# Performance work log

Measured on AMD Instinct MI355X. Metric: run time of the kernel, lower is better.

Reference implementation:

```python
import jax, jax.numpy as jnp
import numpy as np

COST_CLASS = 1.0
COST_BBOX = 5.0
COST_GIOU = 2.0
EPS = 1e-6

BS, Q, T = 8, 900, 256   # batch, num_queries, max_text_len
M = 2000                 # total target boxes concatenated over batch


def setup_inputs() -> dict:
    key = jax.random.key(0)
    k1, k2, k3, k4 = jax.random.split(key, 4)
    pred_logits = jax.random.normal(k1, (BS, Q, T), dtype=jnp.float32)
    pred_boxes = jax.random.uniform(k2, (BS, Q, 4), dtype=jnp.float32, minval=0.05, maxval=0.95)
    tgt_boxes = jax.random.uniform(k3, (M, 4), dtype=jnp.float32, minval=0.05, maxval=0.95)
    tgt_labels = jax.random.uniform(k4, (M, T), dtype=jnp.float32)  # positive token map (soft)
    return {"pred_logits": pred_logits, "pred_boxes": pred_boxes,
            "tgt_boxes": tgt_boxes, "tgt_labels": tgt_labels}


def box_cxcywh_to_xyxy(b):
    cx, cy, w, h = b[..., 0], b[..., 1], b[..., 2], b[..., 3]
    return jnp.stack([cx - 0.5 * w, cy - 0.5 * h, cx + 0.5 * w, cy + 0.5 * h], axis=-1)


def generalized_box_iou(boxes1, boxes2):
    # boxes1: [N,4] xyxy, boxes2: [M,4] xyxy -> [N,M] GIoU
    area1 = (boxes1[:, 2] - boxes1[:, 0]) * (boxes1[:, 3] - boxes1[:, 1])
    area2 = (boxes2[:, 2] - boxes2[:, 0]) * (boxes2[:, 3] - boxes2[:, 1])
    lt = jnp.maximum(boxes1[:, None, :2], boxes2[None, :, :2])  # [N,M,2]
    rb = jnp.minimum(boxes1[:, None, 2:], boxes2[None, :, 2:])
    wh = jnp.clip(rb - lt, 0.0)
    inter = wh[..., 0] * wh[..., 1]
    union = area1[:, None] + area2[None, :] - inter
    iou = inter / (union + EPS)
    lt_e = jnp.minimum(boxes1[:, None, :2], boxes2[None, :, :2])
    rb_e = jnp.maximum(boxes1[:, None, 2:], boxes2[None, :, 2:])
    wh_e = jnp.clip(rb_e - lt_e, 0.0)
    area_e = wh_e[..., 0] * wh_e[..., 1]
    return iou - (area_e - union) / (area_e + EPS)


def reference(pred_logits, pred_boxes, tgt_boxes, tgt_labels):
    bs, q, t = pred_logits.shape
    out_prob = jnp.clip(jax.nn.sigmoid(pred_logits.reshape(bs * q, t)), EPS, 1.0 - EPS)
    pred_bbox = pred_boxes.reshape(bs * q, 4)
    # normalized positive token map
    norm_labels = tgt_labels / (jnp.sum(tgt_labels, axis=1, keepdims=True) + EPS)
    # classification cost: -sum_t p[n,t] * map[m,t]  -> [N, M]
    cost_class = -jnp.einsum('nt,mt->nm', out_prob, norm_labels)
    # L1 box cost (cdist p=1) on cxcywh
    cost_bbox = jnp.sum(jnp.abs(pred_bbox[:, None, :] - tgt_boxes[None, :, :]), axis=-1)
    # GIoU cost on xyxy, clamped to >= -1
    giou = generalized_box_iou(box_cxcywh_to_xyxy(pred_bbox), box_cxcywh_to_xyxy(tgt_boxes))
    cost_giou = -jnp.clip(giou, -1.0)
    C = COST_BBOX * cost_bbox + COST_CLASS * cost_class + COST_GIOU * cost_giou
    return C.reshape(bs, q, -1)
```

## Files before the change

### kernel.cpp

```cpp
#include <hip/hip_runtime.h>
#include <math.h>

#define EPSF 1e-6f

typedef __attribute__((ext_vector_type(8))) short bf16x8;
typedef __attribute__((ext_vector_type(4))) float f32x4;
typedef __attribute__((ext_vector_type(4))) unsigned short u16x4;
typedef __attribute__((ext_vector_type(8))) unsigned short u16x8;

constexpr int TT = 256, MT = 2000, NP = 7200;

static __device__ __forceinline__ unsigned short f2bf(float f) {
    unsigned int u = __float_as_uint(f);
    u += 0x7FFFu + ((u >> 16) & 1u);
    return (unsigned short)(u >> 16);
}
static __device__ __forceinline__ float frcp(float x) { return __builtin_amdgcn_rcpf(x); }

__global__ __launch_bounds__(256) void sigmoid_bf16_kernel(const float* __restrict__ in,
                                                           unsigned short* __restrict__ out) {
    int i = (blockIdx.x * 256 + threadIdx.x) * 8;
    float4 x0 = *reinterpret_cast<const float4*>(in + i);
    float4 x1 = *reinterpret_cast<const float4*>(in + i + 4);
    float v[8] = {x0.x, x0.y, x0.z, x0.w, x1.x, x1.y, x1.z, x1.w};
    u16x8 o;
#pragma unroll
    for (int j = 0; j < 8; ++j) {
        float s = frcp(1.0f + __expf(-v[j]));
        s = fminf(fmaxf(s, EPSF), 1.0f - EPSF);
        o[j] = f2bf(s);
    }
    *reinterpret_cast<u16x8*>(out + i) = o;
}

__global__ __launch_bounds__(256) void normlab_bf16_kernel(const float* __restrict__ lab,
                                                           unsigned short* __restrict__ out) {
    int wave = threadIdx.x >> 6;
    int lane = threadIdx.x & 63;
    int m = blockIdx.x * 4 + wave;
    float4 v = reinterpret_cast<const float4*>(lab)[m * (TT / 4) + lane];
    float s = v.x + v.y + v.z + v.w;
#pragma unroll
    for (int off = 32; off > 0; off >>= 1) s += __shfl_down(s, off);
    float inv = frcp(__shfl(s, 0) + EPSF);
    u16x4 o;
    o[0] = f2bf(v.x * inv); o[1] = f2bf(v.y * inv);
    o[2] = f2bf(v.z * inv); o[3] = f2bf(v.w * inv);
    *reinterpret_cast<u16x4*>(out + m * TT + lane * 4) = o;
}

constexpr int BN = 128, BM = 128, BK = 64;
constexpr int LDT = BK + 8;

__global__ __launch_bounds__(256) void cost_mfma_kernel(
    const unsigned short* __restrict__ A,
    const unsigned short* __restrict__ B,
    const float* __restrict__ pbox,
    const float* __restrict__ tbox,
    float* __restrict__ out)
{
    __shared__ __align__(16) unsigned short As[BN * LDT];
    __shared__ __align__(16) unsigned short Bs[BM * LDT];
    const int tid = threadIdx.x;
    const int n0 = blockIdx.x * BN;
    const int m0 = blockIdx.y * BM;
    const int lane = tid & 63, wave = tid >> 6;
    const int wr = wave & 1, wc = wave >> 1;
    const int fr = lane & 15, quad = lane >> 4;
    const int sc = tid & 7;
    const int sr = tid >> 3;

    f32x4 acc[4][4] = {};

    for (int k0 = 0; k0 < TT; k0 += BK) {
        __syncthreads();
#pragma unroll
        for (int p = 0; p < 4; ++p) {
            int row = sr + p * 32;
            int gn = n0 + row; if (gn > NP - 1) gn = NP - 1;
            bf16x8 va = *reinterpret_cast<const bf16x8*>(&A[gn * TT + k0 + sc * 8]);
            *reinterpret_cast<bf16x8*>(&As[row * LDT + sc * 8]) = va;
            int gm = m0 + row; if (gm > MT - 1) gm = MT - 1;
            bf16x8 vb = *reinterpret_cast<const bf16x8*>(&B[gm * TT + k0 + sc * 8]);
            *reinterpret_cast<bf16x8*>(&Bs[row * LDT + sc * 8]) = vb;
        }
        __syncthreads();
#pragma unroll
        for (int ks = 0; ks < 2; ++ks) {
            bf16x8 af[4], bf[4];
#pragma unroll
            for (int t = 0; t < 4; ++t) {
                af[t] = *reinterpret_cast<const bf16x8*>(
                    &As[(wr * 64 + t * 16 + fr) * LDT + ks * 32 + quad * 8]);
                bf[t] = *reinterpret_cast<const bf16x8*>(
                    &Bs[(wc * 64 + t * 16 + fr) * LDT + ks * 32 + quad * 8]);
            }
#pragma unroll
            for (int ti = 0; ti < 4; ++ti)
#pragma unroll
                for (int tj = 0; tj < 4; ++tj)
                    acc[ti][tj] = __builtin_amdgcn_mfma_f32_16x16x32_bf16(
                        af[ti], bf[tj], acc[ti][tj], 0, 0, 0);
        }
    }

    float bcx[4], bcy[4], bww[4], bhh[4], bx1[4], by1[4], bx2[4], by2[4], areaB[4];
    int mj[4]; bool mv[4];
#pragma unroll
    for (int tj = 0; tj < 4; ++tj) {
        int gm = m0 + wc * 64 + tj * 16 + fr;
        mv[tj] = gm < MT;
        int g = mv[tj] ? gm : MT - 1;
        float4 b = *reinterpret_cast<const float4*>(&tbox[g * 4]);
        bcx[tj] = b.x; bcy[tj] = b.y; bww[tj] = b.z; bhh[tj] = b.w;
        bx1[tj] = b.x - 0.5f * b.z; by1[tj] = b.y - 0.5f * b.w;
        bx2[tj] = b.x + 0.5f * b.z; by2[tj] = b.y + 0.5f * b.w;
        areaB[tj] = (bx2[tj] - bx1[tj]) * (by2[tj] - by1[tj]);
        mj[tj] = gm;
    }

#pragma unroll
    for (int ti = 0; ti < 4; ++ti) {
#pragma unroll
        for (int r = 0; r < 4; ++r) {
            int p = n0 + wr * 64 + ti * 16 + quad * 4 + r;
            if (p >= NP) continue;
            float4 pb = *reinterpret_cast<const float4*>(&pbox[p * 4]);
            float ax1 = pb.x - 0.5f * pb.z, ay1 = pb.y - 0.5f * pb.w;
            float ax2 = pb.x + 0.5f * pb.z, ay2 = pb.y + 0.5f * pb.w;
            float areaA = (ax2 - ax1) * (ay2 - ay1);
#pragma unroll
            for (int tj = 0; tj < 4; ++tj) {
                if (!mv[tj]) continue;
                float l1 = fabsf(pb.x - bcx[tj]) + fabsf(pb.y - bcy[tj]) +
                           fabsf(pb.z - bww[tj]) + fabsf(pb.w - bhh[tj]);
                float ltx = fmaxf(ax1, bx1[tj]), lty = fmaxf(ay1, by1[tj]);
                float rbx = fminf(ax2, bx2[tj]), rby = fminf(ay2, by2[tj]);
                float iw = fmaxf(rbx - ltx, 0.0f), ih = fmaxf(rby - lty, 0.0f);
                float inter = iw * ih;
                float uni = areaA + areaB[tj] - inter;
                float iou = inter * frcp(uni + EPSF);
                float ex1 = fminf(ax1, bx1[tj]), ey1 = fminf(ay1, by1[tj]);
                float ex2 = fmaxf(ax2, bx2[tj]), ey2 = fmaxf(ay2, by2[tj]);
                float ew = fmaxf(ex2 - ex1, 0.0f), eh = fmaxf(ey2 - ey1, 0.0f);
                float areaE = ew * eh;
                float giou = iou - (areaE - uni) * frcp(areaE + EPSF);
                float res = 5.0f * l1 - acc[ti][tj][r] - 2.0f * fmaxf(giou, -1.0f);
                out[p * MT + mj[tj]] = res;
            }
        }
    }
}

extern "C" void kernel_launch(void* const* d_in, const int* in_sizes, int n_in,
                              void* d_out, int out_size, void* d_ws, size_t ws_size,
                              hipStream_t stream) {
    const float* pred_logits = (const float*)d_in[0];
    const float* pred_boxes  = (const float*)d_in[1];
    const float* tgt_boxes   = (const float*)d_in[2];
    const float* tgt_labels  = (const float*)d_in[3];
    float* out = (float*)d_out;

    unsigned short* probs = (unsigned short*)d_ws;
    unsigned short* nlab  = probs + NP * TT;

    sigmoid_bf16_kernel<<<NP * TT / (256 * 8), 256, 0, stream>>>(pred_logits, probs);
    normlab_bf16_kernel<<<MT / 4, 256, 0, stream>>>(tgt_labels, nlab);

    dim3 grid((NP + BN - 1) / BN, (MT + BM - 1) / BM);
    cost_mfma_kernel<<<grid, 256, 0, stream>>>(probs, nlab, pred_boxes, tgt_boxes, out);
}
```

Before: 128.4 us.

## Merge prep kernels and load MFMA operands directly from global memory

Folds the sigmoid and label-normalisation kernels into one launch using block-index ranges, removing one kernel launch. The GEMM main loop drops LDS staging and the two barriers per K-step, and instead has each wave load its MFMA fragments straight from global memory through per-row pointers. This avoids shared-memory traffic and synchronisation but makes the 16-byte fragment loads strided across rows and duplicated between waves, so it leans on L1/L2 caching. The GIoU code also picks up a redundant, odd self-referential ey2 expression that is immediately overwritten.

```diff
diff --git a/kernel.cpp b/kernel.cpp
--- a/kernel.cpp
+++ b/kernel.cpp
@@ -17,40 +17,41 @@
 }
 static __device__ __forceinline__ float frcp(float x) { return __builtin_amdgcn_rcpf(x); }
 
-__global__ __launch_bounds__(256) void sigmoid_bf16_kernel(const float* __restrict__ in,
-                                                           unsigned short* __restrict__ out) {
-    int i = (blockIdx.x * 256 + threadIdx.x) * 8;
-    float4 x0 = *reinterpret_cast<const float4*>(in + i);
-    float4 x1 = *reinterpret_cast<const float4*>(in + i + 4);
-    float v[8] = {x0.x, x0.y, x0.z, x0.w, x1.x, x1.y, x1.z, x1.w};
-    u16x8 o;
+__global__ __launch_bounds__(256) void prep_kernel(const float* __restrict__ logits,
+                                                   const float* __restrict__ lab,
+                                                   unsigned short* __restrict__ probs,
+                                                   unsigned short* __restrict__ nlab) {
+    int b = blockIdx.x;
+    if (b < 900) {
+        int i = (b * 256 + threadIdx.x) * 8;
+        float4 x0 = *reinterpret_cast<const float4*>(logits + i);
+        float4 x1 = *reinterpret_cast<const float4*>(logits + i + 4);
+        float v[8] = {x0.x, x0.y, x0.z, x0.w, x1.x, x1.y, x1.z, x1.w};
+        u16x8 o;
 #pragma unroll
-    for (int j = 0; j < 8; ++j) {
-        float s = frcp(1.0f + __expf(-v[j]));
-        s = fminf(fmaxf(s, EPSF), 1.0f - EPSF);
-        o[j] = f2bf(s);
+        for (int j = 0; j < 8; ++j) {
+            float s = frcp(1.0f + __expf(-v[j]));
+            s = fminf(fmaxf(s, EPSF), 1.0f - EPSF);
+            o[j] = f2bf(s);
+        }
+        *reinterpret_cast<u16x8*>(probs + i) = o;
+    } else {
+        int wave = threadIdx.x >> 6;
+        int lane = threadIdx.x & 63;
+        int m = (b - 900) * 4 + wave;
+        float4 v = reinterpret_cast<const float4*>(lab)[m * (TT / 4) + lane];
+        float s = v.x + v.y + v.z + v.w;
+#pragma unroll
+        for (int off = 32; off > 0; off >>= 1) s += __shfl_down(s, off);
+        float inv = frcp(__shfl(s, 0) + EPSF);
+        u16x4 o;
+        o[0] = f2bf(v.x * inv); o[1] = f2bf(v.y * inv);
+        o[2] = f2bf(v.z * inv); o[3] = f2bf(v.w * inv);
+        *reinterpret_cast<u16x4*>(nlab + m * TT + lane * 4) = o;
     }
-    *reinterpret_cast<u16x8*>(out + i) = o;
 }
 
-__global__ __launch_bounds__(256) void normlab_bf16_kernel(const float* __restrict__ lab,
-                                                           unsigned short* __restrict__ out) {
-    int wave = threadIdx.x >> 6;
-    int lane = threadIdx.x & 63;
-    int m = blockIdx.x * 4 + wave;
-    float4 v = reinterpret_cast<const float4*>(lab)[m * (TT / 4) + lane];
-    float s = v.x + v.y + v.z + v.w;
-#pragma unroll
-    for (int off = 32; off > 0; off >>= 1) s += __shfl_down(s, off);
-    float inv = frcp(__shfl(s, 0) + EPSF);
-    u16x4 o;
-    o[0] = f2bf(v.x * inv); o[1] = f2bf(v.y * inv);
-    o[2] = f2bf(v.z * inv); o[3] = f2bf(v.w * inv);
-    *reinterpret_cast<u16x4*>(out + m * TT + lane * 4) = o;
-}
-
-constexpr int BN = 128, BM = 128, BK = 64;
-constexpr int LDT = BK + 8;
+constexpr int BN = 128, BM = 128;
 
 __global__ __launch_bounds__(256) void cost_mfma_kernel(
     const unsigned short* __restrict__ A,
@@ -59,49 +60,38 @@
     const float* __restrict__ tbox,
     float* __restrict__ out)
 {
-    __shared__ __align__(16) unsigned short As[BN * LDT];
-    __shared__ __align__(16) unsigned short Bs[BM * LDT];
     const int tid = threadIdx.x;
     const int n0 = blockIdx.x * BN;
     const int m0 = blockIdx.y * BM;
     const int lane = tid & 63, wave = tid >> 6;
     const int wr = wave & 1, wc = wave >> 1;
     const int fr = lane & 15, quad = lane >> 4;
-    const int sc = tid & 7;
-    const int sr = tid >> 3;
+
+    const unsigned short* pa[4];
+    const unsigned short* pb[4];
+#pragma unroll
+    for (int t = 0; t < 4; ++t) {
+        int gn = n0 + wr * 64 + t * 16 + fr; if (gn > NP - 1) gn = NP - 1;
+        pa[t] = A + gn * TT + quad * 8;
+        int gm = m0 + wc * 64 + t * 16 + fr; if (gm > MT - 1) gm = MT - 1;
+        pb[t] = B + gm * TT + quad * 8;
+    }
 
     f32x4 acc[4][4] = {};
-
-    for (int k0 = 0; k0 < TT; k0 += BK) {
-        __syncthreads();
+#pragma unroll 2
+    for (int kk = 0; kk < TT; kk += 32) {
+        bf16x8 af[4], bg[4];
 #pragma unroll
-        for (int p = 0; p < 4; ++p) {
-            int row = sr + p * 32;
-            int gn = n0 + row; if (gn > NP - 1) gn = NP - 1;
-            bf16x8 va = *reinterpret_cast<const bf16x8*>(&A[gn * TT + k0 + sc * 8]);
-            *reinterpret_cast<bf16x8*>(&As[row * LDT + sc * 8]) = va;
-            int gm = m0 + row; if (gm > MT - 1) gm = MT - 1;
-            bf16x8 vb = *reinterpret_cast<const bf16x8*>(&B[gm * TT + k0 + sc * 8]);
-            *reinterpret_cast<bf16x8*>(&Bs[row * LDT + sc * 8]) = vb;
+        for (int t = 0; t < 4; ++t) {
+            af[t] = *reinterpret_cast<const bf16x8*>(pa[t] + kk);
+            bg[t] = *reinterpret_cast<const bf16x8*>(pb[t] + kk);
         }
-        __syncthreads();
 #pragma unroll
-        for (int ks = 0; ks < 2; ++ks) {
-            bf16x8 af[4], bf[4];
+        for (int ti = 0; ti < 4; ++ti)
 #pragma unroll
-            for (int t = 0; t < 4; ++t) {
-                af[t] = *reinterpret_cast<const bf16x8*>(
-                    &As[(wr * 64 + t * 16 + fr) * LDT + ks * 32 + quad * 8]);
-                bf[t] = *reinterpret_cast<const bf16x8*>(
-                    &Bs[(wc * 64 + t * 16 + fr) * LDT + ks * 32 + quad * 8]);
-            }
-#pragma unroll
-            for (int ti = 0; ti < 4; ++ti)
-#pragma unroll
-                for (int tj = 0; tj < 4; ++tj)
-                    acc[ti][tj] = __builtin_amdgcn_mfma_f32_16x16x32_bf16(
-                        af[ti], bf[tj], acc[ti][tj], 0, 0, 0);
-        }
+            for (int tj = 0; tj < 4; ++tj)
+                acc[ti][tj] = __builtin_amdgcn_mfma_f32_16x16x32_bf16(
+                    af[ti], bg[tj], acc[ti][tj], 0, 0, 0);
     }
 
     float bcx[4], bcy[4], bww[4], bhh[4], bx1[4], by1[4], bx2[4], by2[4], areaB[4];
@@ -125,15 +115,15 @@
         for (int r = 0; r < 4; ++r) {
             int p = n0 + wr * 64 + ti * 16 + quad * 4 + r;
             if (p >= NP) continue;
-            float4 pb = *reinterpret_cast<const float4*>(&pbox[p * 4]);
-            float ax1 = pb.x - 0.5f * pb.z, ay1 = pb.y - 0.5f * pb.w;
-            float ax2 = pb.x + 0.5f * pb.z, ay2 = pb.y + 0.5f * pb.w;
+            float4 pb4 = *reinterpret_cast<const float4*>(&pbox[p * 4]);
+            float ax1 = pb4.x - 0.5f * pb4.z, ay1 = pb4.y - 0.5f * pb4.w;
+            float ax2 = pb4.x + 0.5f * pb4.z, ay2 = pb4.y + 0.5f * pb4.w;
             float areaA = (ax2 - ax1) * (ay2 - ay1);
 #pragma unroll
             for (int tj = 0; tj < 4; ++tj) {
                 if (!mv[tj]) continue;
-                float l1 = fabsf(pb.x - bcx[tj]) + fabsf(pb.y - bcy[tj]) +
-                           fabsf(pb.z - bww[tj]) + fabsf(pb.w - bhh[tj]);
+                float l1 = fabsf(pb4.x - bcx[tj]) + fabsf(pb4.y - bcy[tj]) +
+                           fabsf(pb4.z - bww[tj]) + fabsf(pb4.w - bhh[tj]);
                 float ltx = fmaxf(ax1, bx1[tj]), lty = fmaxf(ay1, by1[tj]);
                 float rbx = fminf(ax2, bx2[tj]), rby = fminf(ay2, by2[tj]);
                 float iw = fmaxf(rbx - ltx, 0.0f), ih = fmaxf(rby - lty, 0.0f);
@@ -141,7 +131,8 @@
                 float uni = areaA + areaB[tj] - inter;
                 float iou = inter * frcp(uni + EPSF);
                 float ex1 = fminf(ax1, bx1[tj]), ey1 = fminf(ay1, by1[tj]);
-                float ex2 = fmaxf(ax2, bx2[tj]), ey2 = fmaxf(ay2, by2[tj]);
+                float ex2 = fmaxf(ax2, bx2[tj]), ey2 = fmaxf(ey2 = ay2 > by2[tj] ? ay2 : by2[tj], ey2);
+                ex2 = fmaxf(ax2, bx2[tj]); ey2 = fmaxf(ay2, by2[tj]);
                 float ew = fmaxf(ex2 - ex1, 0.0f), eh = fmaxf(ey2 - ey1, 0.0f);
                 float areaE = ew * eh;
                 float giou = iou - (areaE - uni) * frcp(areaE + EPSF);
@@ -164,8 +155,7 @@
     unsigned short* probs = (unsigned short*)d_ws;
     unsigned short* nlab  = probs + NP * TT;
 
-    sigmoid_bf16_kernel<<<NP * TT / (256 * 8), 256, 0, stream>>>(pred_logits, probs);
-    normlab_bf16_kernel<<<MT / 4, 256, 0, stream>>>(tgt_labels, nlab);
+    prep_kernel<<<900 + 500, 256, 0, stream>>>(pred_logits, tgt_labels, probs, nlab);
 
     dim3 grid((NP + BN - 1) / BN, (MT + BM - 1) / BM);
     cost_mfma_kernel<<<grid, 256, 0, stream>>>(probs, nlab, pred_boxes, tgt_boxes, out);
```

Measured after the change: 134.0 us. 4.4% more time.
